# Performance work log

Hardware: AMD Instinct MI355X
Metric: run time of the kernel (lower is better)

## Reference

```python
import jax, jax.numpy as jnp
import numpy as np

DIM, DH, H_HEADS, F, HH, WW = 512, 64, 8, 16, 32, 32
FF_IN = int(DIM * 4 * 2 / 3)  # 1365


def _ln(x, w, b):
    m = x.mean(-1, keepdims=True)
    v = ((x - m) ** 2).mean(-1, keepdims=True)
    return (x - m) * jax.lax.rsqrt(v + 1e-5) * w + b


def _attn(x, ln_w, ln_b, wq, wkv, nkv, nbias, wout, oln_w, oln_b, rel_bias):
    # x: (B, N, D); K/V are single-head (shared across heads) per the source to_kv
    B, N, D = x.shape
    H = nbias.shape[0]
    dh = nkv.shape[-1]
    xn = _ln(x, ln_w, ln_b)
    q = (xn @ wq).reshape(B, N, H, dh).transpose(0, 2, 1, 3) * (dh ** -0.5)
    k, v = jnp.split(xn @ wkv, 2, axis=-1)  # (B, N, dh) each
    nk = jnp.broadcast_to(nkv[0], (B, 1, dh))
    nv = jnp.broadcast_to(nkv[1], (B, 1, dh))
    k = jnp.concatenate([nk, k], axis=1)  # (B, N+1, dh)
    v = jnp.concatenate([nv, v], axis=1)
    sim = jnp.einsum('bhid,bjd->bhij', q, k)  # (B, H, N, N+1)
    bias = jnp.concatenate([jnp.broadcast_to(nbias[:, None, None], (H, N, 1)), rel_bias], axis=-1)
    attn = jax.nn.softmax(sim + bias[None], axis=-1)
    out = jnp.einsum('bhij,bjd->bhid', attn, v)
    out = out.transpose(0, 2, 1, 3).reshape(B, N, H * dh)
    return _ln(out @ wout, oln_w, oln_b)


def _cpb_mlp(coords, w0, b0, w1, b1, w2, b2):
    t = jax.nn.silu(coords @ w0 + b0)
    t = jax.nn.silu(t @ w1 + b1)
    return t @ w2 + b2  # (R, heads)


def _spatial_bias(h, w, w0, b0, w1, b1, w2, b2):
    rh = jnp.arange(-h + 1, h)
    rw = jnp.arange(-w + 1, w)
    gh, gw = jnp.meshgrid(rh, rw, indexing='ij')
    coords = jnp.stack([gh, gw], axis=-1).reshape(-1, 2).astype(jnp.float32)
    table = _cpb_mlp(coords, w0, b0, w1, b1, w2, b2)  # ((2h-1)(2w-1), H)
    ph, pw = jnp.meshgrid(jnp.arange(h), jnp.arange(w), indexing='ij')
    p = jnp.stack([ph, pw], axis=-1).reshape(-1, 2)  # (hw, 2)
    rel = p[:, None] - p[None]  # (hw, hw, 2)
    idx = (rel[..., 0] + h - 1) * (2 * w - 1) + (rel[..., 1] + w - 1)
    return table[idx].transpose(2, 0, 1)  # (H, hw, hw)


def _temporal_bias(f, w0, b0, w1, b1, w2, b2):
    coords = jnp.arange(-f + 1, f, dtype=jnp.float32)[:, None]
    table = _cpb_mlp(coords, w0, b0, w1, b1, w2, b2)  # (2f-1, H)
    idx = jnp.arange(f)[:, None] - jnp.arange(f)[None] + f - 1
    return table[idx].transpose(2, 0, 1)  # (H, f, f)


def _ff(x, win, g, wout):
    # 1x1x1 conv == channel matmul; GEGLU; shift_token; ChanLayerNorm; conv out
    y = jnp.einsum('bcfhw,cd->bdfhw', x, win)
    a, gate = jnp.split(y, 2, axis=1)
    y = a * jax.nn.gelu(gate, approximate=False)
    c = y.shape[1]
    c1 = (c + 1) // 2  # torch.chunk: first chunk gets ceil
    y1, y2 = y[:, :c1], y[:, c1:]
    y2 = jnp.pad(y2, ((0, 0), (0, 0), (1, 0), (0, 0), (0, 0)))[:, :, :-1]
    y = jnp.concatenate([y1, y2], axis=1)
    m = y.mean(1, keepdims=True)
    v = ((y - m) ** 2).mean(1, keepdims=True)
    y = (y - m) * jax.lax.rsqrt(jnp.maximum(v, 1e-5)) * g.reshape(1, -1, 1, 1, 1)
    return jnp.einsum('bcfhw,cd->bdfhw', y, wout)


def setup_inputs() -> dict:
    key = jax.random.key(0)
    ks = jax.random.split(key, 32)
    d2 = DIM // 2
    inner = DH * H_HEADS

    def nrm(k, shape, s=0.02):
        return jax.random.normal(k, shape, jnp.float32) * s

    inp = {'x': jax.random.normal(ks[0], (1, DIM, F, HH, WW), jnp.float32)}
    for pre, i in (('sa', 1), ('ta', 11)):
        inp[pre + '_ln_w'] = jnp.ones(DIM, jnp.float32)
        inp[pre + '_ln_b'] = jnp.zeros(DIM, jnp.float32)
        inp[pre + '_wq'] = nrm(ks[i], (DIM, inner))
        inp[pre + '_wkv'] = nrm(ks[i + 1], (DIM, 2 * DH))
        inp[pre + '_null_kv'] = nrm(ks[i + 2], (2, DH), 1.0)
        inp[pre + '_null_bias'] = nrm(ks[i + 3], (H_HEADS,), 1.0)
        inp[pre + '_wout'] = nrm(ks[i + 4], (inner, DIM))
        inp[pre + '_oln_w'] = jnp.ones(DIM, jnp.float32)
        inp[pre + '_oln_b'] = jnp.zeros(DIM, jnp.float32)
    inp['sp_w0'] = nrm(ks[20], (2, d2), 0.1); inp['sp_b0'] = jnp.zeros(d2, jnp.float32)
    inp['sp_w1'] = nrm(ks[21], (d2, d2), 0.05); inp['sp_b1'] = jnp.zeros(d2, jnp.float32)
    inp['sp_w2'] = nrm(ks[22], (d2, H_HEADS), 0.05); inp['sp_b2'] = jnp.zeros(H_HEADS, jnp.float32)
    inp['tp_w0'] = nrm(ks[23], (1, d2), 0.1); inp['tp_b0'] = jnp.zeros(d2, jnp.float32)
    inp['tp_w1'] = nrm(ks[24], (d2, d2), 0.05); inp['tp_b1'] = jnp.zeros(d2, jnp.float32)
    inp['tp_w2'] = nrm(ks[25], (d2, H_HEADS), 0.05); inp['tp_b2'] = jnp.zeros(H_HEADS, jnp.float32)
    inp['ff_win'] = nrm(ks[26], (DIM, 2 * FF_IN))
    inp['ff_g'] = jnp.ones(FF_IN, jnp.float32)
    inp['ff_wout'] = nrm(ks[27], (FF_IN, DIM))
    return inp


def _forward(x, sa_ln_w, sa_ln_b, sa_wq, sa_wkv, sa_null_kv, sa_null_bias, sa_wout, sa_oln_w, sa_oln_b,
             ta_ln_w, ta_ln_b, ta_wq, ta_wkv, ta_null_kv, ta_null_bias, ta_wout, ta_oln_w, ta_oln_b,
             sp_w0, sp_b0, sp_w1, sp_b1, sp_w2, sp_b2,
             tp_w0, tp_b0, tp_w1, tp_b1, tp_w2, tp_b2,
             ff_win, ff_g, ff_wout):
    b, c, f, h, w = x.shape
    # spatial attention over (h*w) tokens, batched over (b*f)
    xs = x.transpose(0, 2, 3, 4, 1).reshape(b * f, h * w, c)
    sb = _spatial_bias(h, w, sp_w0, sp_b0, sp_w1, sp_b1, sp_w2, sp_b2)
    xs = _attn(xs, sa_ln_w, sa_ln_b, sa_wq, sa_wkv, sa_null_kv, sa_null_bias, sa_wout, sa_oln_w, sa_oln_b, sb) + xs
    xv = xs.reshape(b, f, h, w, c).transpose(0, 4, 1, 2, 3)
    # temporal attention over f tokens, batched over (b*h*w)
    xt = xv.transpose(0, 3, 4, 2, 1).reshape(b * h * w, f, c)
    tb = _temporal_bias(f, tp_w0, tp_b0, tp_w1, tp_b1, tp_w2, tp_b2)
    xt = _attn(xt, ta_ln_w, ta_ln_b, ta_wq, ta_wkv, ta_null_kv, ta_null_bias, ta_wout, ta_oln_w, ta_oln_b, tb) + xt
    xv = xt.reshape(b, h, w, f, c).transpose(0, 4, 3, 1, 2)
    # feed-forward with token shift
    return _ff(xv, ff_win, ff_g, ff_wout) + xv


def reference(x, sa_ln_w, sa_ln_b, sa_wq, sa_wkv, sa_null_kv, sa_null_bias, sa_wout, sa_oln_w, sa_oln_b,
              ta_ln_w, ta_ln_b, ta_wq, ta_wkv, ta_null_kv, ta_null_bias, ta_wout, ta_oln_w, ta_oln_b,
              sp_w0, sp_b0, sp_w1, sp_b1, sp_w2, sp_b2,
              tp_w0, tp_b0, tp_w1, tp_b1, tp_w2, tp_b2,
              ff_win, ff_g, ff_wout):
    return _forward(x, sa_ln_w, sa_ln_b, sa_wq, sa_wkv, sa_null_kv, sa_null_bias, sa_wout, sa_oln_w, sa_oln_b,
                    ta_ln_w, ta_ln_b, ta_wq, ta_wkv, ta_null_kv, ta_null_bias, ta_wout, ta_oln_w, ta_oln_b,
                    sp_w0, sp_b0, sp_w1, sp_b1, sp_w2, sp_b2,
                    tp_w0, tp_b0, tp_w1, tp_b1, tp_w2, tp_b2,
                    ff_win, ff_g, ff_wout)
```

## Files before the change

### kernel.cpp

```cpp
#include <hip/hip_runtime.h>
#include <math.h>

#define TOK 16384
#define DIMC 512
#define FFI 1365
#define CH1 683
#define YSLD 1376
#define KVPAD 1056
#define BSTRIDE 1152
#define MASKB (-30000.f)
#define LOG2E 1.4426950408889634f

typedef unsigned int u32;
typedef unsigned short ushort_t;
typedef __attribute__((ext_vector_type(8))) short bf16x8;
typedef __attribute__((ext_vector_type(4))) float f32x4;

__device__ inline ushort_t f2b(float x) {
    u32 u = __float_as_uint(x);
    u32 r = (u + 0x7fffu + ((u >> 16) & 1u)) >> 16;
    return (ushort_t)r;
}
__device__ inline float b2f(ushort_t u) { return __uint_as_float(((u32)u) << 16); }

__device__ inline float exp2_fast(float x) {
    float r;
    asm("v_exp_f32 %0, %1" : "=v"(r) : "v"(x));
    return r;
}

__device__ inline u32 cvt_pk_bf16(float lo, float hi) {
    u32 r;
    asm("v_cvt_pk_bf16_f32 %0, %1, %2" : "=v"(r) : "v"(lo), "v"(hi));
    return r;
}

__device__ inline void gload_lds16(const void* g, void* l) {
    __builtin_amdgcn_global_load_lds(
        (const __attribute__((address_space(1))) u32*)g,
        (__attribute__((address_space(3))) u32*)l, 16, 0, 0);
}

__device__ inline float gelu_exact(float x) {
    return 0.5f * x * (1.f + erff(x * 0.70710678118654752f));
}

__global__ __launch_bounds__(256) void cpb_kernel(
    const float* __restrict__ w0, const float* __restrict__ b0,
    const float* __restrict__ w1, const float* __restrict__ b1,
    const float* __restrict__ w2, const float* __restrict__ b2,
    float* __restrict__ table, int mode)
{
    __shared__ float t0[256];
    __shared__ float t1[256];
    int r = blockIdx.x;
    int t = threadIdx.x;
    float c0, c1;
    if (mode == 0) { c0 = (float)(r / 63 - 31); c1 = (float)(r % 63 - 31); }
    else           { c0 = (float)(r - 15);      c1 = 0.f; }
    float a = c0 * w0[t] + b0[t];
    if (mode == 0) a += c1 * w0[256 + t];
    t0[t] = a / (1.f + __expf(-a));
    __syncthreads();
    float s = b1[t];
    for (int k = 0; k < 256; ++k) s += t0[k] * w1[k * 256 + t];
    t1[t] = s / (1.f + __expf(-s));
    __syncthreads();
    if (t < 8) {
        float o = b2[t];
        for (int k = 0; k < 256; ++k) o += t1[k] * w2[k * 8 + t];
        table[r * 8 + t] = o;
    }
}

__global__ __launch_bounds__(256) void bias_sp_kernel(
    const float* __restrict__ tab, const float* __restrict__ nullbias,
    ushort_t* __restrict__ out)
{
    int pi = blockIdx.x, h = blockIdx.y;
    int phi = pi >> 5, pwi = pi & 31;
    ushort_t* row = out + ((size_t)h * 1024 + pi) * BSTRIDE;
    for (int c = threadIdx.x; c < BSTRIDE; c += 256) {
        float v;
        if (c == 0) v = nullbias[h];
        else if (c <= 1024) {
            int pj = c - 1;
            int phj = pj >> 5, pwj = pj & 31;
            int idx = (phi - phj + 31) * 63 + (pwi - pwj + 31);
            v = tab[idx * 8 + h];
        } else v = MASKB;
        row[c] = f2b(v * LOG2E);
    }
}

__global__ __launch_bounds__(256) void kvinit_kernel(
    const float* __restrict__ nullkv, ushort_t* __restrict__ KP, ushort_t* __restrict__ VT)
{
    int f = blockIdx.x, t = threadIdx.x;
    for (int e = t; e < 32 * 64; e += 256) {
        int rr = e >> 6, d = e & 63;
        int row = (rr == 0) ? 0 : (1024 + rr);
        KP[((size_t)f * KVPAD + row) * 64 + d] = (rr == 0) ? f2b(nullkv[d]) : (ushort_t)0;
    }
    for (int e = t; e < 64 * 32; e += 256) {
        int d = e >> 5, cc = e & 31;
        int col = (cc == 0) ? 0 : (1024 + cc);
        VT[((size_t)f * 64 + d) * KVPAD + col] = (cc == 0) ? f2b(nullkv[64 + d]) : (ushort_t)0;
    }
}

__global__ __launch_bounds__(256) void wcvt_kernel(
    const float* __restrict__ W, int ldw, int c0,
    ushort_t* __restrict__ Bt, int Kp, int K, int Ncols,
    const float* __restrict__ gv, int Nwrite)
{
    __shared__ float tile[32][33];
    int nb = blockIdx.x * 32, kb = blockIdx.y * 32;
    int tx = threadIdx.x & 31, ty = threadIdx.x >> 5;
    #pragma unroll
    for (int it = 0; it < 4; ++it) {
        int k = kb + ty + it * 8, n = nb + tx;
        float v = (k < K && n < Ncols) ? W[(size_t)k * ldw + c0 + n] : 0.f;
        if (gv && k < K) v *= gv[k];
        tile[ty + it * 8][tx] = v;
    }
    __syncthreads();
    #pragma unroll
    for (int it = 0; it < 4; ++it) {
        int n = nb + ty + it * 8, k = kb + tx;
        if (n < Nwrite && k < Kp) Bt[(size_t)n * Kp + k] = f2b(tile[tx][ty + it * 8]);
    }
}

__global__ __launch_bounds__(256) void transpose_in_kernel(
    const float* __restrict__ x, float* __restrict__ dst)
{
    __shared__ float tile[32][33];
    int t0b = blockIdx.x * 32, c0b = blockIdx.y * 32;
    int tx = threadIdx.x & 31, ty = threadIdx.x >> 5;
    #pragma unroll
    for (int it = 0; it < 4; ++it) {
        int c = ty + it * 8;
        tile[c][tx] = x[(size_t)(c0b + c) * TOK + t0b + tx];
    }
    __syncthreads();
    #pragma unroll
    for (int it = 0; it < 4; ++it) {
        int tr = ty + it * 8;
        dst[(size_t)(t0b + tr) * DIMC + c0b + tx] = tile[tx][tr];
    }
}

__global__ __launch_bounds__(256) void ln_bf16_kernel(
    const float* __restrict__ in, ushort_t* __restrict__ out,
    const float* __restrict__ w, const float* __restrict__ b)
{
    __shared__ float r1[4], r2[4];
    size_t base = (size_t)blockIdx.x * DIMC;
    int t = threadIdx.x;
    float x0 = in[base + t], x1 = in[base + 256 + t];
    float s = x0 + x1, s2 = x0 * x0 + x1 * x1;
    #pragma unroll
    for (int o = 32; o > 0; o >>= 1) { s += __shfl_down(s, o, 64); s2 += __shfl_down(s2, o, 64); }
    if ((t & 63) == 0) { r1[t >> 6] = s; r2[t >> 6] = s2; }
    __syncthreads();
    float mean = (r1[0] + r1[1] + r1[2] + r1[3]) * (1.f / 512.f);
    float ex2  = (r2[0] + r2[1] + r2[2] + r2[3]) * (1.f / 512.f);
    float rstd = rsqrtf(ex2 - mean * mean + 1e-5f);
    out[base + t]       = f2b((x0 - mean) * rstd * w[t] + b[t]);
    out[base + 256 + t] = f2b((x1 - mean) * rstd * w[256 + t] + b[256 + t]);
}

__global__ __launch_bounds__(256) void ln_add_kernel(
    const float* __restrict__ proj, float* __restrict__ io,
    const float* __restrict__ w, const float* __restrict__ b)
{
    __shared__ float r1[4], r2[4];
    size_t base = (size_t)blockIdx.x * DIMC;
    int t = threadIdx.x;
    float x0 = proj[base + t], x1 = proj[base + 256 + t];
    float s = x0 + x1, s2 = x0 * x0 + x1 * x1;
    #pragma unroll
    for (int o = 32; o > 0; o >>= 1) { s += __shfl_down(s, o, 64); s2 += __shfl_down(s2, o, 64); }
    if ((t & 63) == 0) { r1[t >> 6] = s; r2[t >> 6] = s2; }
    __syncthreads();
    float mean = (r1[0] + r1[1] + r1[2] + r1[3]) * (1.f / 512.f);
    float ex2  = (r2[0] + r2[1] + r2[2] + r2[3]) * (1.f / 512.f);
    float rstd = rsqrtf(ex2 - mean * mean + 1e-5f);
    io[base + t]       += (x0 - mean) * rstd * w[t] + b[t];
    io[base + 256 + t] += (x1 - mean) * rstd * w[256 + t] + b[256 + t];
}

__global__ __launch_bounds__(128) void permute0_kernel(
    const float* __restrict__ src, float* __restrict__ dst)
{
    int rd = blockIdx.x;
    int rs = (rd & 15) * 1024 + (rd >> 4);
    ((float4*)(dst + (size_t)rd * DIMC))[threadIdx.x] =
        ((const float4*)(src + (size_t)rs * DIMC))[threadIdx.x];
}

__global__ __launch_bounds__(128) void permute1_dual_kernel(
    const float* __restrict__ src, float* __restrict__ dst, ushort_t* __restrict__ dstb)
{
    int rd = blockIdx.x;
    int rs = (rd & 1023) * 16 + (rd >> 10);
    float4 v = ((const float4*)(src + (size_t)rs * DIMC))[threadIdx.x];
    ((float4*)(dst + (size_t)rd * DIMC))[threadIdx.x] = v;
    u32 lo = (u32)f2b(v.x) | ((u32)f2b(v.y) << 16);
    u32 hi = (u32)f2b(v.z) | ((u32)f2b(v.w) << 16);
    ((uint2*)(dstb + (size_t)rd * DIMC))[threadIdx.x] = make_uint2(lo, hi);
}

template<int EPI>
__global__ __launch_bounds__(256) void gemm_mfma(
    const ushort_t* __restrict__ A, int lda,
    const ushort_t* __restrict__ Bt, int Kp,
    float* __restrict__ C, ushort_t* __restrict__ Cb, int ldc,
    int M, int N, int K, float scale, int nx,
    const float* __restrict__ stats, const float* __restrict__ g,
    const float* __restrict__ resid, float* __restrict__ outT,
    ushort_t* __restrict__ KPo, ushort_t* __restrict__ VTo)
{
    __shared__ __align__(16) ushort_t As[2][4 * 128 * 8];
    __shared__ __align__(16) ushort_t Bs[2][4 * 128 * 8];
    int lin = blockIdx.x;
    int xcd = lin & 7, idx = lin >> 3;
    int m0 = (xcd * 16 + (idx & 15)) * 128;
    int n0 = (idx >> 4) * 128;
    int tid = threadIdx.x, lane = tid & 63, wid = tid >> 6;
    int wy = wid >> 1, wx = wid & 1, quad = lane >> 4, l16 = lane & 15;
    bool bfull = (n0 + 128 <= N);
    f32x4 acc[4][4];
    #pragma unroll
    for (int i = 0; i < 4; ++i)
        #pragma unroll
        for (int j = 0; j < 4; ++j) { acc[i][j][0]=0.f; acc[i][j][1]=0.f; acc[i][j][2]=0.f; acc[i][j][3]=0.f; }

    auto stage = [&](int buf, int k0) {
        #pragma unroll
        for (int r = 0; r < 2; ++r) {
            int c = wid * 128 + r * 64 + lane;
            const ushort_t* src = A + (size_t)(m0 + (c & 127)) * lda + k0 + (c >> 7) * 8;
            gload_lds16(src, &As[buf][(wid * 128 + r * 64) * 8]);
        }
        if (bfull) {
            #pragma unroll
            for (int r = 0; r < 2; ++r) {
                int c = wid * 128 + r * 64 + lane;
                const ushort_t* src = Bt + (size_t)(n0 + (c & 127)) * Kp + k0 + (c >> 7) * 8;
                gload_lds16(src, &Bs[buf][(wid * 128 + r * 64) * 8]);
            }
        } else {
            #pragma unroll
            for (int r = 0; r < 2; ++r) {
                int c = tid + r * 256;
                int kg = c >> 7, nloc = c & 127;
                bf16x8 v;
                if (n0 + nloc < N) v = *(const bf16x8*)(Bt + (size_t)(n0 + nloc) * Kp + k0 + kg * 8);
                else { for (int e = 0; e < 8; ++e) v[e] = 0; }
                *(bf16x8*)&Bs[buf][c * 8] = v;
            }
        }
    };

    stage(0, 0);
    __syncthreads();
    for (int k0 = 0; k0 < K; k0 += 32) {
        int cur = (k0 >> 5) & 1;
        if (k0 + 32 < K) stage(cur ^ 1, k0 + 32);
        bf16x8 af[4], bfr[4];
        #pragma unroll
        for (int i = 0; i < 4; ++i) af[i] = *(bf16x8*)&As[cur][(quad * 128 + wy * 64 + i * 16 + l16) * 8];
        #pragma unroll
        for (int j = 0; j < 4; ++j) bfr[j] = *(bf16x8*)&Bs[cur][(quad * 128 + wx * 64 + j * 16 + l16) * 8];
        #pragma unroll
        for (int i = 0; i < 4; ++i)
            #pragma unroll
            for (int j = 0; j < 4; ++j)
                acc[i][j] = __builtin_amdgcn_mfma_f32_16x16x32_bf16(af[i], bfr[j], acc[i][j], 0, 0, 0);
        __syncthreads();
    }
    #pragma unroll
    for (int i = 0; i < 4; ++i) {
        #pragma unroll
        for (int j = 0; j < 4; ++j) {
            #pragma unroll
            for (int r = 0; r < 4; ++r) {
                int m = m0 + wy * 64 + i * 16 + quad * 4 + r;
                int n = n0 + wx * 64 + j * 16 + l16;
                if (n >= N) continue;
                float v = acc[i][j][r] * scale;
                if (EPI == 0) {
                    C[(size_t)m * ldc + n] = v;
                } else if (EPI == 3) {
                    Cb[(size_t)m * ldc + n] = f2b(v);
                } else if (EPI == 4) {
                    int frame = m >> 10, tt = m & 1023;
                    if (n < 64) KPo[((size_t)frame * KVPAD + 1 + tt) * 64 + n] = f2b(v);
                    else        VTo[((size_t)frame * 64 + (n - 64)) * KVPAD + 1 + tt] = f2b(v);
                } else if (EPI == 5) {
                    float s0 = stats[2 * m], s1 = stats[2 * m + 1];
                    outT[(size_t)n * TOK + m] = v * s1 - s0 * g[n] + resid[(size_t)m * DIMC + n];
                }
            }
        }
    }
}

__global__ __launch_bounds__(256) void ff_gemm_fused(
    const ushort_t* __restrict__ A,
    const ushort_t* __restrict__ BI,
    ushort_t* __restrict__ YS)
{
    __shared__ __align__(16) ushort_t As[2][4 * 128 * 8];
    __shared__ __align__(16) ushort_t Bs[2][4 * 2 * 64 * 8];
    int lin = blockIdx.x;
    int xcd = lin & 7, idx = lin >> 3;
    int m0 = (xcd * 16 + (idx & 15)) * 128;
    int n0 = (idx >> 4) * 64;
    int tid = threadIdx.x, lane = tid & 63, wid = tid >> 6;
    int wy = wid >> 1, wx = wid & 1, quad = lane >> 4, l16 = lane & 15;
    f32x4 aA[4][2], aG[4][2];
    #pragma unroll
    for (int i = 0; i < 4; ++i)
        #pragma unroll
        for (int j = 0; j < 2; ++j) {
            aA[i][j][0]=0.f; aA[i][j][1]=0.f; aA[i][j][2]=0.f; aA[i][j][3]=0.f;
            aG[i][j][0]=0.f; aG[i][j][1]=0.f; aG[i][j][2]=0.f; aG[i][j][3]=0.f;
        }

    auto stage = [&](int buf, int k0) {
        #pragma unroll
        for (int r = 0; r < 2; ++r) {
            int c = wid * 128 + r * 64 + lane;
            gload_lds16(A + (size_t)(m0 + (c & 127)) * 512 + k0 + (c >> 7) * 8,
                        &As[buf][(wid * 128 + r * 64) * 8]);
        }
        #pragma unroll
        for (int r = 0; r < 2; ++r) {
            gload_lds16(BI + (size_t)((n0 + lane) * 2 + r) * 512 + k0 + wid * 8,
                        &Bs[buf][(wid * 128 + r * 64) * 8]);
        }
    };

    stage(0, 0);
    __syncthreads();
    for (int k0 = 0; k0 < 512; k0 += 32) {
        int cur = (k0 >> 5) & 1;
        if (k0 + 32 < 512) stage(cur ^ 1, k0 + 32);
        bf16x8 af[4], ba[2], bg[2];
        #pragma unroll
        for (int i = 0; i < 4; ++i) af[i] = *(bf16x8*)&As[cur][(quad * 128 + wy * 64 + i * 16 + l16) * 8];
        #pragma unroll
        for (int j = 0; j < 2; ++j) {
            int nn = wx * 32 + j * 16 + l16;
            ba[j] = *(bf16x8*)&Bs[cur][(quad * 128 + nn) * 8];
            bg[j] = *(bf16x8*)&Bs[cur][(quad * 128 + 64 + nn) * 8];
        }
        #pragma unroll
        for (int i = 0; i < 4; ++i)
            #pragma unroll
            for (int j = 0; j < 2; ++j) {
                aA[i][j] = __builtin_amdgcn_mfma_f32_16x16x32_bf16(af[i], ba[j], aA[i][j], 0, 0, 0);
                aG[i][j] = __builtin_amdgcn_mfma_f32_16x16x32_bf16(af[i], bg[j], aG[i][j], 0, 0, 0);
            }
        __syncthreads();
    }
    #pragma unroll
    for (int i = 0; i < 4; ++i) {
        #pragma unroll
        for (int j = 0; j < 2; ++j) {
            #pragma unroll
            for (int r = 0; r < 4; ++r) {
                int m = m0 + wy * 64 + i * 16 + quad * 4 + r;
                int n = n0 + wx * 32 + j * 16 + l16;
                if (n >= FFI) {
                    if (n < YSLD) YS[(size_t)m * YSLD + n] = 0;
                    continue;
                }
                float v = aA[i][j][r] * gelu_exact(aG[i][j][r]);
                int dr = (n < CH1) ? m : m + 1024;
                if (dr < TOK) YS[(size_t)dr * YSLD + n] = f2b(v);
                if (n >= CH1 && m < 1024) YS[(size_t)m * YSLD + n] = 0;
            }
        }
    }
}

__global__ __launch_bounds__(256) void attn_sp_mfma(
    const ushort_t* __restrict__ Q,
    const ushort_t* __restrict__ KP,
    const ushort_t* __restrict__ VT,
    const ushort_t* __restrict__ BIASX,
    ushort_t* __restrict__ O)
{
    __shared__ __align__(16) ushort_t Ks[128 * 64];
    __shared__ __align__(16) ushort_t Vs[64 * 128];
    int lin = blockIdx.x;
    int xcd = lin & 7, idx = lin >> 3;
    int qt = xcd * 8 + (idx & 7);
    int frame = idx >> 3;
    int q0 = qt * 16;
    int tid = threadIdx.x, lane = tid & 63, wid = tid >> 6;
    int quad = lane >> 4, l16 = lane & 15;

    bf16x8 aQ[2][2];
    const ushort_t* brow[2];
    #pragma unroll
    for (int i = 0; i < 2; ++i) {
        int h = wid * 2 + i;
        const ushort_t* qp = Q + (size_t)(frame * 1024 + q0 + l16) * 512 + h * 64 + quad * 8;
        aQ[i][0] = *(const bf16x8*)qp;
        aQ[i][1] = *(const bf16x8*)(qp + 32);
        brow[i] = BIASX + ((size_t)h * 1024 + q0 + l16) * BSTRIDE;
    }
    f32x4 Oc[2][4];
    f32x4 Oc4[2];
    #pragma unroll
    for (int i = 0; i < 2; ++i) {
        #pragma unroll
        for (int nt = 0; nt < 4; ++nt) { Oc[i][nt][0]=0.f; Oc[i][nt][1]=0.f; Oc[i][nt][2]=0.f; Oc[i][nt][3]=0.f; }
        Oc4[i][0]=0.f; Oc4[i][1]=0.f; Oc4[i][2]=0.f; Oc4[i][3]=0.f;
    }
    bf16x8 vones;
    #pragma unroll
    for (int e = 0; e < 8; ++e) vones[e] = (short)0x3F80;

    int idxA = (((quad & 1) * 32) + l16) * 4;
    int idxB = idxA + 64;
    bool hiq = (quad >= 2);

    for (int jt = 0; jt < 9; ++jt) {
        __syncthreads();
        #pragma unroll
        for (int r = 0; r < 4; ++r) {
            int L = wid * 256 + r * 64 + lane;
            int c = L >> 3, gp = L & 7, gg = gp ^ (c & 7);
            int jj = jt * 128 + c; if (jj > KVPAD - 1) jj = KVPAD - 1;
            gload_lds16(KP + ((size_t)frame * KVPAD + jj) * 64 + gg * 8, &Ks[(wid * 256 + r * 64) * 8]);
        }
        #pragma unroll
        for (int r = 0; r < 4; ++r) {
            int L = wid * 256 + r * 64 + lane;
            int d = L >> 4, cgp = L & 15;
            int cg = (cgp & 8) | ((cgp & 7) ^ (d & 7));
            int col = jt * 128 + cg * 8; if (col > KVPAD - 8) col = KVPAD - 8;
            gload_lds16(VT + ((size_t)frame * 64 + d) * KVPAD + col, &Vs[(wid * 256 + r * 64) * 8]);
        }
        __syncthreads();

        #pragma unroll
        for (int i = 0; i < 2; ++i) {
            f32x4 S[8];
            #pragma unroll
            for (int j = 0; j < 8; ++j) { S[j][0]=0.f; S[j][1]=0.f; S[j][2]=0.f; S[j][3]=0.f; }
            __builtin_amdgcn_s_setprio(1);
            #pragma unroll
            for (int j = 0; j < 8; ++j) {
                int c = j * 16 + l16;
                #pragma unroll
                for (int ks = 0; ks < 2; ++ks) {
                    bf16x8 kb = *(bf16x8*)&Ks[(c * 8 + ((ks * 4 + quad) ^ (c & 7))) * 8];
                    S[j] = __builtin_amdgcn_mfma_f32_16x16x32_bf16(kb, aQ[i][ks], S[j], 0, 0, 0);
                }
            }
            __builtin_amdgcn_s_setprio(0);
            #pragma unroll
            for (int j = 0; j < 8; ++j) {
                int kbase = jt * 128 + j * 16 + quad * 4;
                uint2 bv = *(const uint2*)(brow[i] + kbase);
                S[j][0] = exp2_fast(S[j][0] + __uint_as_float(bv.x << 16));
                S[j][1] = exp2_fast(S[j][1] + __uint_as_float(bv.x & 0xffff0000u));
                S[j][2] = exp2_fast(S[j][2] + __uint_as_float(bv.y << 16));
                S[j][3] = exp2_fast(S[j][3] + __uint_as_float(bv.y & 0xffff0000u));
            }
            __builtin_amdgcn_s_setprio(1);
            #pragma unroll
            for (int ks = 0; ks < 4; ++ks) {
                int jl = 2 * ks, jh = 2 * ks + 1;
                u32 pxl = cvt_pk_bf16(S[jl][0], S[jl][1]);
                u32 pyl = cvt_pk_bf16(S[jl][2], S[jl][3]);
                u32 pxh = cvt_pk_bf16(S[jh][0], S[jh][1]);
                u32 pyh = cvt_pk_bf16(S[jh][2], S[jh][3]);
                u32 a0 = (u32)__builtin_amdgcn_ds_bpermute(idxA, (int)pxl);
                u32 a1 = (u32)__builtin_amdgcn_ds_bpermute(idxA, (int)pxh);
                u32 b0 = (u32)__builtin_amdgcn_ds_bpermute(idxA, (int)pyl);
                u32 b1 = (u32)__builtin_amdgcn_ds_bpermute(idxA, (int)pyh);
                u32 c0 = (u32)__builtin_amdgcn_ds_bpermute(idxB, (int)pxl);
                u32 c1 = (u32)__builtin_amdgcn_ds_bpermute(idxB, (int)pxh);
                u32 d0 = (u32)__builtin_amdgcn_ds_bpermute(idxB, (int)pyl);
                u32 d1 = (u32)__builtin_amdgcn_ds_bpermute(idxB, (int)pyh);
                union { u32 w[4]; bf16x8 v; } pa;
                pa.w[0] = hiq ? a1 : a0;
                pa.w[1] = hiq ? b1 : b0;
                pa.w[2] = hiq ? c1 : c0;
                pa.w[3] = hiq ? d1 : d0;
                #pragma unroll
                for (int nt = 0; nt < 4; ++nt) {
                    int d = nt * 16 + l16;
                    int cg = ks * 4 + quad;
                    int phys = (cg & 8) | ((cg & 7) ^ (d & 7));
                    bf16x8 vb = *(bf16x8*)&Vs[(d * 16 + phys) * 8];
                    Oc[i][nt] = __builtin_amdgcn_mfma_f32_16x16x32_bf16(pa.v, vb, Oc[i][nt], 0, 0, 0);
                }
                Oc4[i] = __builtin_amdgcn_mfma_f32_16x16x32_bf16(pa.v, vones, Oc4[i], 0, 0, 0);
            }
            __builtin_amdgcn_s_setprio(0);
        }
    }
    #pragma unroll
    for (int i = 0; i < 2; ++i) {
        int h = wid * 2 + i;
        #pragma unroll
        for (int r = 0; r < 4; ++r) {
            float linv = 1.f / Oc4[i][r];
            int ql = quad * 4 + r;
            #pragma unroll
            for (int nt = 0; nt < 4; ++nt) {
                int d = nt * 16 + l16;
                O[(size_t)(frame * 1024 + q0 + ql) * 512 + h * 64 + d] = f2b(Oc[i][nt][r] * linv);
            }
        }
    }
}

__global__ __launch_bounds__(256) void attn_tp_kernel(
    const ushort_t* __restrict__ q, const ushort_t* __restrict__ kv,
    const float* __restrict__ nullkv, const float* __restrict__ nullbias,
    const float* __restrict__ table, ushort_t* __restrict__ out)
{
    __shared__ float qs[16][512];
    __shared__ float ks[17][64];
    __shared__ float vs[17][64];
    __shared__ float sc[8][16][17];
    int b = blockIdx.x;
    int t = threadIdx.x;
    for (int e = t; e < 16 * 512; e += 256) {
        int f = e >> 9, c = e & 511;
        qs[f][c] = b2f(q[(size_t)(b * 16 + f) * 512 + c]);
    }
    for (int e = t; e < 17 * 64; e += 256) {
        int j = e >> 6, d = e & 63;
        ks[j][d] = (j == 0) ? nullkv[d]      : b2f(kv[(size_t)(b * 16 + j - 1) * 128 + d]);
        vs[j][d] = (j == 0) ? nullkv[64 + d] : b2f(kv[(size_t)(b * 16 + j - 1) * 128 + 64 + d]);
    }
    __syncthreads();
    for (int e = t; e < 8 * 16 * 17; e += 256) {
        int h = e / 272, rem = e - h * 272;
        int i = rem / 17, j = rem - i * 17;
        float acc = 0.f;
        for (int d = 0; d < 64; ++d) acc += qs[i][h * 64 + d] * ks[j][d];
        float bias = ((j == 0) ? nullbias[h] : table[(i - (j - 1) + 15) * 8 + h]) * LOG2E;
        sc[h][i][j] = acc + bias;
    }
    __syncthreads();
    if (t < 128) {
        int h = t >> 4, i = t & 15;
        float mx = -1e30f;
        for (int j = 0; j < 17; ++j) mx = fmaxf(mx, sc[h][i][j]);
        float s = 0.f;
        for (int j = 0; j < 17; ++j) { float p = exp2_fast(sc[h][i][j] - mx); sc[h][i][j] = p; s += p; }
        float inv = 1.f / s;
        for (int j = 0; j < 17; ++j) sc[h][i][j] *= inv;
    }
    __syncthreads();
    for (int e = t; e < 16 * 512; e += 256) {
        int i = e >> 9, c = e & 511;
        int h = c >> 6, d = c & 63;
        float acc = 0.f;
        #pragma unroll
        for (int j = 0; j < 17; ++j) acc += sc[h][i][j] * vs[j][d];
        out[(size_t)(b * 16 + i) * 512 + c] = f2b(acc);
    }
}

__global__ __launch_bounds__(256) void rowstats_bf16_kernel(
    const ushort_t* __restrict__ YS, float* __restrict__ stats)
{
    __shared__ float r1[4], r2[4];
    int r = blockIdx.x, t = threadIdx.x;
    const ushort_t* row = YS + (size_t)r * YSLD;
    float s = 0.f, s2 = 0.f;
    for (int c = t; c < FFI; c += 256) {
        float v = b2f(row[c]);
        s += v; s2 += v * v;
    }
    #pragma unroll
    for (int o = 32; o > 0; o >>= 1) { s += __shfl_down(s, o, 64); s2 += __shfl_down(s2, o, 64); }
    if ((t & 63) == 0) { r1[t >> 6] = s; r2[t >> 6] = s2; }
    __syncthreads();
    float S  = r1[0] + r1[1] + r1[2] + r1[3];
    float S2 = r2[0] + r2[1] + r2[2] + r2[3];
    float mean = S * (1.f / 1365.f);
    float var  = S2 * (1.f / 1365.f) - mean * mean;
    float rstd = rsqrtf(fmaxf(var, 1e-5f));
    if (t == 0) { stats[2 * r] = mean * rstd; stats[2 * r + 1] = rstd; }
}

__global__ __launch_bounds__(64) void colsum_kernel(
    const ushort_t* __restrict__ Wt, float* __restrict__ colsum)
{
    int n = blockIdx.x, t = threadIdx.x;
    const ushort_t* row = Wt + (size_t)n * YSLD;
    float s = 0.f;
    for (int k = t; k < YSLD; k += 64) s += b2f(row[k]);
    #pragma unroll
    for (int o = 32; o > 0; o >>= 1) s += __shfl_down(s, o, 64);
    if (t == 0) colsum[n] = s;
}

extern "C" void kernel_launch(void* const* d_in, const int* in_sizes, int n_in,
                              void* d_out, int out_size, void* d_ws, size_t ws_size,
                              hipStream_t stream)
{
    const float* x          = (const float*)d_in[0];
    const float* sa_ln_w    = (const float*)d_in[1];
    const float* sa_ln_b    = (const float*)d_in[2];
    const float* sa_wq      = (const float*)d_in[3];
    const float* sa_wkv     = (const float*)d_in[4];
    const float* sa_null_kv = (const float*)d_in[5];
    const float* sa_null_b  = (const float*)d_in[6];
    const float* sa_wout    = (const float*)d_in[7];
    const float* sa_oln_w   = (const float*)d_in[8];
    const float* sa_oln_b   = (const float*)d_in[9];
    const float* ta_ln_w    = (const float*)d_in[10];
    const float* ta_ln_b    = (const float*)d_in[11];
    const float* ta_wq      = (const float*)d_in[12];
    const float* ta_wkv     = (const float*)d_in[13];
    const float* ta_null_kv = (const float*)d_in[14];
    const float* ta_null_b  = (const float*)d_in[15];
    const float* ta_wout    = (const float*)d_in[16];
    const float* ta_oln_w   = (const float*)d_in[17];
    const float* ta_oln_b   = (const float*)d_in[18];
    const float* sp_w0      = (const float*)d_in[19];
    const float* sp_b0      = (const float*)d_in[20];
    const float* sp_w1      = (const float*)d_in[21];
    const float* sp_b1      = (const float*)d_in[22];
    const float* sp_w2      = (const float*)d_in[23];
    const float* sp_b2      = (const float*)d_in[24];
    const float* tp_w0      = (const float*)d_in[25];
    const float* tp_b0      = (const float*)d_in[26];
    const float* tp_w1      = (const float*)d_in[27];
    const float* tp_b1      = (const float*)d_in[28];
    const float* tp_w2      = (const float*)d_in[29];
    const float* tp_b2      = (const float*)d_in[30];
    const float* ff_win     = (const float*)d_in[31];
    const float* ff_g       = (const float*)d_in[32];
    const float* ff_wout    = (const float*)d_in[33];

    char* ws = (char*)d_ws;
    float*    RES   = (float*)(ws + 0);
    ushort_t* XN16  = (ushort_t*)(ws + 33554432);
    ushort_t* Q16   = (ushort_t*)(ws + 50331648);
    float*    RT    = (float*)(ws + 50331648);
    ushort_t* YS    = (ushort_t*)(ws + 50331648);
    ushort_t* WSA   = (ushort_t*)(ws + 67108864);
    ushort_t* KP    = (ushort_t*)(ws + 83886080);
    ushort_t* VTb   = (ushort_t*)(ws + 86048768);
    ushort_t* KV16  = (ushort_t*)(ws + 83886080);
    ushort_t* WTA   = (ushort_t*)(ws + 90439680);
    ushort_t* AO16  = (ushort_t*)(ws + 92274688);
    ushort_t* BI    = (ushort_t*)(ws + 96468992);
    ushort_t* WFFB  = (ushort_t*)(ws + 99352576);
    ushort_t* BIAS16= (ushort_t*)(ws + 109051904);
    float*    PRJ   = (float*)(ws + 109051904);
    ushort_t* Q16t  = (ushort_t*)(ws + 109051904);
    float*    STATS = (float*)(ws + 142606336);
    float*    SPT   = (float*)(ws + 142737408);
    float*    COLSUM= (float*)(ws + 142737408);
    float*    TPT   = (float*)(ws + 142864448);

    ushort_t* WQ_T  = WSA;
    ushort_t* WKV_T = WSA + 262144;
    ushort_t* WO_T  = WSA + 327680;
    ushort_t* tWQ_T  = WTA;
    ushort_t* tWKV_T = WTA + 262144;
    ushort_t* tWO_T  = WTA + 327680;

    dim3 blk(256);
    const float QSCL = 0.125f * LOG2E;

    cpb_kernel<<<dim3(3969), blk, 0, stream>>>(sp_w0, sp_b0, sp_w1, sp_b1, sp_w2, sp_b2, SPT, 0);
    cpb_kernel<<<dim3(31),   blk, 0, stream>>>(tp_w0, tp_b0, tp_w1, tp_b1, tp_w2, tp_b2, TPT, 1);
    bias_sp_kernel<<<dim3(1024, 8), blk, 0, stream>>>(SPT, sa_null_b, BIAS16);
    kvinit_kernel<<<dim3(16), blk, 0, stream>>>(sa_null_kv, KP, VTb);

    wcvt_kernel<<<dim3(16, 16), blk, 0, stream>>>(sa_wq, 512, 0, WQ_T, 512, 512, 512, nullptr, 512);
    wcvt_kernel<<<dim3(4, 16),  blk, 0, stream>>>(sa_wkv, 128, 0, WKV_T, 512, 512, 128, nullptr, 128);
    wcvt_kernel<<<dim3(16, 16), blk, 0, stream>>>(sa_wout, 512, 0, WO_T, 512, 512, 512, nullptr, 512);
    transpose_in_kernel<<<dim3(512, 16), blk, 0, stream>>>(x, RES);
    ln_bf16_kernel<<<dim3(TOK), blk, 0, stream>>>(RES, XN16, sa_ln_w, sa_ln_b);
    gemm_mfma<3><<<dim3(512), blk, 0, stream>>>(XN16, 512, WQ_T, 512,
        nullptr, Q16, 512, TOK, 512, 512, QSCL, 4, nullptr, nullptr, nullptr, nullptr, nullptr, nullptr);
    gemm_mfma<4><<<dim3(128), blk, 0, stream>>>(XN16, 512, WKV_T, 512,
        nullptr, nullptr, 0, TOK, 128, 512, 1.0f, 1, nullptr, nullptr, nullptr, nullptr, KP, VTb);
    attn_sp_mfma<<<dim3(1024), blk, 0, stream>>>(Q16, KP, VTb, BIAS16, AO16);
    gemm_mfma<0><<<dim3(512), blk, 0, stream>>>(AO16, 512, WO_T, 512,
        PRJ, nullptr, 512, TOK, 512, 512, 1.0f, 4, nullptr, nullptr, nullptr, nullptr, nullptr, nullptr);
    ln_add_kernel<<<dim3(TOK), blk, 0, stream>>>(PRJ, RES, sa_oln_w, sa_oln_b);

    permute0_kernel<<<dim3(TOK), dim3(128), 0, stream>>>(RES, RT);
    wcvt_kernel<<<dim3(16, 16), blk, 0, stream>>>(ta_wq, 512, 0, tWQ_T, 512, 512, 512, nullptr, 512);
    wcvt_kernel<<<dim3(4, 16),  blk, 0, stream>>>(ta_wkv, 128, 0, tWKV_T, 512, 512, 128, nullptr, 128);
    wcvt_kernel<<<dim3(16, 16), blk, 0, stream>>>(ta_wout, 512, 0, tWO_T, 512, 512, 512, nullptr, 512);
    ln_bf16_kernel<<<dim3(TOK), blk, 0, stream>>>(RT, XN16, ta_ln_w, ta_ln_b);
    gemm_mfma<3><<<dim3(512), blk, 0, stream>>>(XN16, 512, tWQ_T, 512,
        nullptr, Q16t, 512, TOK, 512, 512, QSCL, 4, nullptr, nullptr, nullptr, nullptr, nullptr, nullptr);
    gemm_mfma<3><<<dim3(128), blk, 0, stream>>>(XN16, 512, tWKV_T, 512,
        nullptr, KV16, 128, TOK, 128, 512, 1.0f, 1, nullptr, nullptr, nullptr, nullptr, nullptr, nullptr);
    attn_tp_kernel<<<dim3(1024), blk, 0, stream>>>(Q16t, KV16, ta_null_kv, ta_null_b, TPT, AO16);
    gemm_mfma<0><<<dim3(512), blk, 0, stream>>>(AO16, 512, tWO_T, 512,
        PRJ, nullptr, 512, TOK, 512, 512, 1.0f, 4, nullptr, nullptr, nullptr, nullptr, nullptr, nullptr);
    ln_add_kernel<<<dim3(TOK), blk, 0, stream>>>(PRJ, RT, ta_oln_w, ta_oln_b);
    permute1_dual_kernel<<<dim3(TOK), dim3(128), 0, stream>>>(RT, RES, XN16);

    wcvt_kernel<<<dim3(44, 16), blk, 0, stream>>>(ff_win, 2730, 0,   BI,       1024, 512, FFI, nullptr, 1408);
    wcvt_kernel<<<dim3(44, 16), blk, 0, stream>>>(ff_win, 2730, FFI, BI + 512, 1024, 512, FFI, nullptr, 1408);
    wcvt_kernel<<<dim3(16, 43), blk, 0, stream>>>(ff_wout, 512, 0, WFFB, YSLD, FFI, 512, ff_g, 512);
    colsum_kernel<<<dim3(512), dim3(64), 0, stream>>>(WFFB, COLSUM);
    ff_gemm_fused<<<dim3(2816), blk, 0, stream>>>(XN16, BI, YS);
    rowstats_bf16_kernel<<<dim3(TOK), blk, 0, stream>>>(YS, STATS);
    gemm_mfma<5><<<dim3(512), blk, 0, stream>>>(YS, YSLD, WFFB, YSLD,
        nullptr, nullptr, 0, TOK, 512, YSLD, 1.0f, 4, STATS, COLSUM, RES, (float*)d_out, nullptr, nullptr);
}
```

Measured before the change: 860.7 us.

## Pipeline GEMM global-to-LDS loads two stages ahead with explicit vmcnt waits

Restructures the main GEMM and the fused GEGLU GEMM k-loops so that two K-tiles are in flight at once. Explicit s_waitcnt vmcnt(4) plus raw s_barrier calls replace the full __syncthreads drain each iteration, so the next tile's global_load_lds can overlap the MFMAs on the current one. The partial-N path is moved to a simpler single-buffer loop. This relies on the exact count of outstanding vector memory ops per stage (4) and on LDS-read ordering before the buffer is overwritten, which is fragile.

Measured after the change: 843.1 us. -2.0%, faster.

```diff
diff --git a/kernel.cpp b/kernel.cpp
--- a/kernel.cpp
+++ b/kernel.cpp
@@ -43,6 +43,15 @@
 
 __device__ inline float gelu_exact(float x) {
     return 0.5f * x * (1.f + erff(x * 0.70710678118654752f));
+}
+
+__device__ inline void waitcnt_vm4() {
+    asm volatile("s_waitcnt vmcnt(4)" ::: "memory");
+    __builtin_amdgcn_sched_barrier(0);
+}
+__device__ inline void waitcnt_vm0() {
+    asm volatile("s_waitcnt vmcnt(0)" ::: "memory");
+    __builtin_amdgcn_sched_barrier(0);
 }
 
 __global__ __launch_bounds__(256) void cpb_kernel(
@@ -237,21 +246,50 @@
         #pragma unroll
         for (int j = 0; j < 4; ++j) { acc[i][j][0]=0.f; acc[i][j][1]=0.f; acc[i][j][2]=0.f; acc[i][j][3]=0.f; }
 
-    auto stage = [&](int buf, int k0) {
+    auto stageA = [&](int buf, int k0) {
         #pragma unroll
         for (int r = 0; r < 2; ++r) {
             int c = wid * 128 + r * 64 + lane;
             const ushort_t* src = A + (size_t)(m0 + (c & 127)) * lda + k0 + (c >> 7) * 8;
             gload_lds16(src, &As[buf][(wid * 128 + r * 64) * 8]);
         }
-        if (bfull) {
-            #pragma unroll
-            for (int r = 0; r < 2; ++r) {
-                int c = wid * 128 + r * 64 + lane;
-                const ushort_t* src = Bt + (size_t)(n0 + (c & 127)) * Kp + k0 + (c >> 7) * 8;
-                gload_lds16(src, &Bs[buf][(wid * 128 + r * 64) * 8]);
-            }
-        } else {
+    };
+    auto stageB = [&](int buf, int k0) {
+        #pragma unroll
+        for (int r = 0; r < 2; ++r) {
+            int c = wid * 128 + r * 64 + lane;
+            const ushort_t* src = Bt + (size_t)(n0 + (c & 127)) * Kp + k0 + (c >> 7) * 8;
+            gload_lds16(src, &Bs[buf][(wid * 128 + r * 64) * 8]);
+        }
+    };
+
+    if (bfull) {
+        int NT = K >> 5;
+        stageA(0, 0); stageB(0, 0);
+        if (NT > 1) { stageA(1, 32); stageB(1, 32); }
+        for (int t = 0; t < NT; ++t) {
+            if (t + 1 < NT) waitcnt_vm4(); else waitcnt_vm0();
+            __builtin_amdgcn_s_barrier();
+            int cur = t & 1;
+            bf16x8 af[4], bfr[4];
+            #pragma unroll
+            for (int i = 0; i < 4; ++i) af[i] = *(bf16x8*)&As[cur][(quad * 128 + wy * 64 + i * 16 + l16) * 8];
+            #pragma unroll
+            for (int j = 0; j < 4; ++j) bfr[j] = *(bf16x8*)&Bs[cur][(quad * 128 + wx * 64 + j * 16 + l16) * 8];
+            #pragma unroll
+            for (int i = 0; i < 4; ++i)
+                #pragma unroll
+                for (int j = 0; j < 4; ++j)
+                    acc[i][j] = __builtin_amdgcn_mfma_f32_16x16x32_bf16(af[i], bfr[j], acc[i][j], 0, 0, 0);
+            if (t + 2 < NT) {
+                __builtin_amdgcn_s_barrier();
+                stageA(cur, (t + 2) * 32); stageB(cur, (t + 2) * 32);
+            }
+        }
+    } else {
+        for (int k0 = 0; k0 < K; k0 += 32) {
+            if (k0) __syncthreads();
+            stageA(0, k0);
             #pragma unroll
             for (int r = 0; r < 2; ++r) {
                 int c = tid + r * 256;
@@ -259,27 +297,20 @@
                 bf16x8 v;
                 if (n0 + nloc < N) v = *(const bf16x8*)(Bt + (size_t)(n0 + nloc) * Kp + k0 + kg * 8);
                 else { for (int e = 0; e < 8; ++e) v[e] = 0; }
-                *(bf16x8*)&Bs[buf][c * 8] = v;
-            }
-        }
-    };
-
-    stage(0, 0);
-    __syncthreads();
-    for (int k0 = 0; k0 < K; k0 += 32) {
-        int cur = (k0 >> 5) & 1;
-        if (k0 + 32 < K) stage(cur ^ 1, k0 + 32);
-        bf16x8 af[4], bfr[4];
-        #pragma unroll
-        for (int i = 0; i < 4; ++i) af[i] = *(bf16x8*)&As[cur][(quad * 128 + wy * 64 + i * 16 + l16) * 8];
-        #pragma unroll
-        for (int j = 0; j < 4; ++j) bfr[j] = *(bf16x8*)&Bs[cur][(quad * 128 + wx * 64 + j * 16 + l16) * 8];
-        #pragma unroll
-        for (int i = 0; i < 4; ++i)
-            #pragma unroll
-            for (int j = 0; j < 4; ++j)
-                acc[i][j] = __builtin_amdgcn_mfma_f32_16x16x32_bf16(af[i], bfr[j], acc[i][j], 0, 0, 0);
-        __syncthreads();
+                *(bf16x8*)&Bs[0][c * 8] = v;
+            }
+            __syncthreads();
+            bf16x8 af[4], bfr[4];
+            #pragma unroll
+            for (int i = 0; i < 4; ++i) af[i] = *(bf16x8*)&As[0][(quad * 128 + wy * 64 + i * 16 + l16) * 8];
+            #pragma unroll
+            for (int j = 0; j < 4; ++j) bfr[j] = *(bf16x8*)&Bs[0][(quad * 128 + wx * 64 + j * 16 + l16) * 8];
+            #pragma unroll
+            for (int i = 0; i < 4; ++i)
+                #pragma unroll
+                for (int j = 0; j < 4; ++j)
+                    acc[i][j] = __builtin_amdgcn_mfma_f32_16x16x32_bf16(af[i], bfr[j], acc[i][j], 0, 0, 0);
+        }
     }
     #pragma unroll
     for (int i = 0; i < 4; ++i) {
@@ -345,10 +376,11 @@
     };
 
     stage(0, 0);
-    __syncthreads();
-    for (int k0 = 0; k0 < 512; k0 += 32) {
-        int cur = (k0 >> 5) & 1;
-        if (k0 + 32 < 512) stage(cur ^ 1, k0 + 32);
+    stage(1, 32);
+    for (int t = 0; t < 16; ++t) {
+        if (t + 1 < 16) waitcnt_vm4(); else waitcnt_vm0();
+        __builtin_amdgcn_s_barrier();
+        int cur = t & 1;
         bf16x8 af[4], ba[2], bg[2];
         #pragma unroll
         for (int i = 0; i < 4; ++i) af[i] = *(bf16x8*)&As[cur][(quad * 128 + wy * 64 + i * 16 + l16) * 8];
@@ -365,7 +397,10 @@
                 aA[i][j] = __builtin_amdgcn_mfma_f32_16x16x32_bf16(af[i], ba[j], aA[i][j], 0, 0, 0);
                 aG[i][j] = __builtin_amdgcn_mfma_f32_16x16x32_bf16(af[i], bg[j], aG[i][j], 0, 0, 0);
             }
-        __syncthreads();
+        if (t + 2 < 16) {
+            __builtin_amdgcn_s_barrier();
+            stage(cur, (t + 2) * 32);
+        }
     }
     #pragma unroll
     for (int i = 0; i < 4; ++i) {
```
